# Performance work log

Measured on AMD Instinct MI355X. Metric: run time of the kernel, lower is better.

Reference implementation:

```python
import jax, jax.numpy as jnp
import numpy as np
from jax import lax

IMG_SIZE = 608
STRIDE = 32
NUM_CLASSES = 20
CONF_THRESH = 0.001
NMS_THRESH = 0.6
SLOPE = 0.1
B = 16
P5 = 512
FMP = IMG_SIZE // STRIDE   # 19
N = FMP * FMP              # 361 boxes per image


def _conv(x, w, b):
    y = lax.conv_general_dilated(x, w, (1, 1), 'SAME',
                                 dimension_numbers=('NCHW', 'OIHW', 'NCHW'))
    return y + b[None, :, None, None]


def _conv_act(x, w, b):
    # Conv block (conv + folded-BN bias + LeakyReLU(0.1)) at inference
    return jax.nn.leaky_relu(_conv(x, w, b), SLOPE)


def _grid():
    gy, gx = jnp.meshgrid(jnp.arange(FMP), jnp.arange(FMP), indexing='ij')
    return jnp.stack([gx, gy], axis=-1).reshape(-1, 2).astype(jnp.float32)  # [N,2]


def _decode(reg):
    # reg: [B,N,4] raw head output -> normalized x1y1x2y2 clamped to [0,1]
    xy = jax.nn.sigmoid(reg[..., :2]) + _grid()[None]          # center_sample=False
    wh = jnp.exp(reg[..., 2:])
    box = jnp.concatenate([xy - wh * 0.5, xy + wh * 0.5], axis=-1)
    return jnp.clip(box * (STRIDE / IMG_SIZE), 0.0, 1.0)


def _nms_one_class(boxes, s):
    # boxes: [N,4]; s: [N] scores with -1 marking boxes not of this class / below conf
    order = jnp.argsort(-s)
    b = boxes[order]
    valid = s[order] >= CONF_THRESH
    x1, y1, x2, y2 = b[:, 0], b[:, 1], b[:, 2], b[:, 3]
    areas = (x2 - x1) * (y2 - y1)
    w = jnp.maximum(1e-28, jnp.minimum(x2[:, None], x2[None, :]) - jnp.maximum(x1[:, None], x1[None, :]))
    h = jnp.maximum(1e-28, jnp.minimum(y2[:, None], y2[None, :]) - jnp.maximum(y1[:, None], y1[None, :]))
    inter = w * h
    iou = inter / (areas[:, None] + areas[None, :] - inter + 1e-14)  # [N,N]
    later = jnp.arange(N)[None, :] > jnp.arange(N)[:, None]
    sup = (iou > NMS_THRESH) & later

    def body(i, keep):
        # box i suppresses later boxes only if itself still kept (greedy NMS)
        return keep & ~(sup[i] & keep[i])

    keep = lax.fori_loop(0, N, body, valid)
    return jnp.zeros(N, dtype=bool).at[order].set(keep)  # back to original order


def _postprocess(boxes, scores):
    # per image: boxes [N,4], scores [N,C]
    cls_inds = jnp.argmax(scores, axis=-1)
    sc = jnp.max(scores, axis=-1)
    cmask = (cls_inds[None, :] == jnp.arange(NUM_CLASSES)[:, None]) & (sc >= CONF_THRESH)[None, :]
    masked = jnp.where(cmask, sc[None, :], -1.0)  # [C,N]
    keep_c = jax.vmap(_nms_one_class, in_axes=(None, 0))(boxes, masked)
    return sc, cls_inds, jnp.any(keep_c, axis=0)


def setup_inputs() -> dict:
    key = jax.random.key(0)
    ks = jax.random.split(key, 16)
    inp = {'x': jax.random.normal(ks[0], (B, P5, FMP, FMP), jnp.float32)}
    names = ['cls1', 'cls2', 'reg1', 'reg2', 'reg3', 'reg4']
    for j, nm in enumerate(names):
        inp['w_' + nm] = jax.random.normal(ks[1 + j], (P5, P5, 3, 3), jnp.float32) * 0.02
        inp['b_' + nm] = jnp.zeros((P5,), jnp.float32)
    inp['w_obj'] = jax.random.normal(ks[8], (1, P5, 1, 1), jnp.float32) * 0.01
    inp['b_obj'] = jnp.zeros((1,), jnp.float32)
    inp['w_clsh'] = jax.random.normal(ks[9], (NUM_CLASSES, P5, 1, 1), jnp.float32) * 0.01
    inp['b_clsh'] = jnp.zeros((NUM_CLASSES,), jnp.float32)
    inp['w_regh'] = jax.random.normal(ks[10], (4, P5, 1, 1), jnp.float32) * 0.01
    inp['b_regh'] = jnp.zeros((4,), jnp.float32)
    return inp


def reference(x, w_cls1, b_cls1, w_cls2, b_cls2, w_reg1, b_reg1, w_reg2, b_reg2,
              w_reg3, b_reg3, w_reg4, b_reg4, w_obj, b_obj, w_clsh, b_clsh,
              w_regh, b_regh):
    cf = _conv_act(_conv_act(x, w_cls1, b_cls1), w_cls2, b_cls2)
    rf = x
    for wv, bv in ((w_reg1, b_reg1), (w_reg2, b_reg2), (w_reg3, b_reg3), (w_reg4, b_reg4)):
        rf = _conv_act(rf, wv, bv)

    def flat(t):  # [B,C,H,W] -> [B,N,C]
        return t.reshape(t.shape[0], t.shape[1], -1).transpose(0, 2, 1)

    obj = flat(_conv(rf, w_obj, b_obj))      # [B,N,1]
    clsp = flat(_conv(cf, w_clsh, b_clsh))   # [B,N,C]
    regp = flat(_conv(rf, w_regh, b_regh))   # [B,N,4]

    boxes = _decode(regp)                                        # [B,N,4]
    scores = jax.nn.sigmoid(obj) * jax.nn.softmax(clsp, axis=-1)  # [B,N,C]
    sc, cls_inds, keep = jax.vmap(_postprocess)(boxes, scores)
    # fixed-shape outputs: boxes [B,N,4], per-box best score [B,N],
    # class index [B,N], NMS keep mask [B,N]
    return boxes, sc, cls_inds, keep
```

## Files before the change

### kernel.cpp

```cpp
#include <hip/hip_runtime.h>
#include <hip/hip_bf16.h>
#include <stdint.h>

typedef __bf16 bf16x8 __attribute__((ext_vector_type(8)));
typedef float  f32x16 __attribute__((ext_vector_type(16)));

#define FMPX 19
#define NPOS 361
#define CCH  512
#define NB   16
#define NCLS 20
#define CONF_T 0.001f
#define NMS_TH 0.6f
#define BSCALE (32.0f/608.0f)

#define SC_OFF   (NB*NPOS*4)
#define CLS_OFF  (SC_OFF + NB*NPOS)
#define KEEP_OFF (CLS_OFF + NB*NPOS)

#define GSTR  3528
#define PLANE ((size_t)3612672)
#define WSL   294912
#define XBUF  16384
#define WOFF  32768
#define SMEMB 51200

__device__ __forceinline__ void gl_lds16(const void* g, void* l) {
  __builtin_amdgcn_global_load_lds(
      (const __attribute__((address_space(1))) unsigned int*)g,
      (__attribute__((address_space(3))) unsigned int*)l, 16, 0, 0);
}
#define MFMA32(A,B,C) __builtin_amdgcn_mfma_f32_32x32x16_bf16(A,B,C,0,0,0)
#define SG(m,n) __builtin_amdgcn_sched_group_barrier(m, n, 0)
#define PRIO1 __builtin_amdgcn_s_setprio(1)
#define PRIO0 __builtin_amdgcn_s_setprio(0)

__global__ void split_x_k(const float* __restrict__ x, __bf16* __restrict__ Xd) {
  __shared__ float sx[8][368];
  int g = blockIdx.x, b = blockIdx.y;
  int tid = threadIdx.x;
  for (int i = tid; i < 8*361; i += 256) {
    int ci = i / 361, p = i - ci*361;
    sx[ci][p] = x[((size_t)b*CCH + g*8 + ci)*NPOS + p];
  }
  __syncthreads();
  for (int row = tid; row < 441; row += 256) {
    int y = row/21, xx = row - y*21;
    bf16x8 oh = {}, om = {};
    if (y >= 1 && y <= 19 && xx >= 1 && xx <= 19) {
      int p = (y-1)*19 + xx - 1;
#pragma unroll
      for (int j = 0; j < 8; ++j) {
        float v = sx[j][p];
        __bf16 hh = (__bf16)v;
        oh[j] = hh; om[j] = (__bf16)(v - (float)hh);
      }
    }
    size_t o = (((size_t)b)*64 + g)*GSTR + (size_t)row*8;
    *(bf16x8*)(Xd + o)         = oh;
    *(bf16x8*)(Xd + PLANE + o) = om;
  }
}

__global__ void repack_k(const float* __restrict__ w, __bf16* __restrict__ Wg) {
  __shared__ float sw[32][145];
  int slice = blockIdx.x, chunk = blockIdx.y;
  int tid = threadIdx.x;
  for (int i = tid; i < 32*144; i += 256) {
    int cl = i / 144, r = i - cl*144;
    sw[cl][r] = w[((size_t)slice*32 + cl)*4608 + chunk*144 + r];
  }
  __syncthreads();
  for (int u = tid; u < 1152; u += 256) {
    int co = u & 31, kh = (u >> 5) & 1, pt = u >> 6;
    int tap = pt % 9, pl = pt / 9;
    bf16x8 o;
#pragma unroll
    for (int j = 0; j < 8; ++j) {
      float v = sw[co][(kh*8 + j)*9 + tap];
      __bf16 hh = (__bf16)v;
      o[j] = pl == 0 ? hh : (__bf16)(v - (float)hh);
    }
    *(bf16x8*)(Wg + (((size_t)(slice*2 + pl)*9 + tap)*32 + chunk)*512 + kh*256 + co*8) = o;
  }
}

#define RD4X(SP, AT, IMM) do { \
  SP##0 = *(const bf16x8*)(Xc + AT##0 + (IMM)); \
  SP##1 = *(const bf16x8*)(Xc + AT##1 + (IMM)); \
  SP##2 = *(const bf16x8*)(Xc + AT##2 + (IMM)); \
  SP##3 = *(const bf16x8*)(Xc + AT##3 + (IMM)); } while (0)

#define CL4(SP, BH_, BM_) do { \
  acc0 = MFMA32(SP##0, BH_, acc0); acc1 = MFMA32(SP##1, BH_, acc1); \
  acc2 = MFMA32(SP##2, BH_, acc2); acc3 = MFMA32(SP##3, BH_, acc3); \
  acc0 = MFMA32(SP##0, BM_, acc0); acc1 = MFMA32(SP##1, BM_, acc1); \
  acc2 = MFMA32(SP##2, BM_, acc2); acc3 = MFMA32(SP##3, BM_, acc3); } while (0)

#define CL4H(SP, B_) do { \
  acc0 = MFMA32(SP##0, B_, acc0); acc1 = MFMA32(SP##1, B_, acc1); \
  acc2 = MFMA32(SP##2, B_, acc2); acc3 = MFMA32(SP##3, B_, acc3); } while (0)

#define STO(A, MTL) do { _Pragma("unroll") \
  for (int r = 0; r < 16; ++r) { \
    Lf[wq*2368 + ((MTL)*32 + 4*kh + (r & 3) + 8*(r >> 2))*37 + col] = (A)[r]; } } while (0)

__global__ __launch_bounds__(256, 3) void conv3x3_mfma(
    const __bf16* __restrict__ Xs, const __bf16* __restrict__ Wg,
    const float* __restrict__ bias, __bf16* __restrict__ Xd)
{
  __shared__ __attribute__((aligned(16))) char smem[SMEMB];
  const int tid = threadIdx.x;
  const int bid = blockIdx.x;
  const int b = bid & 15, slice = (bid >> 4) & 15, h = bid >> 8;
  const int lane = tid & 63;
  const int wq = __builtin_amdgcn_readfirstlane(tid >> 6);
  const int col = lane & 31, kh = lane >> 5;
  const int kh4096 = kh*4096;
  const int PB = h*128, CNT = (h == 2) ? 105 : 128;
  const int PEND = PB + CNT - 1;
  const int wstart = (h == 0) ? 0 : (h == 1) ? 140 : 282;
  const int clampU = (h == 2) ? 158 : 255;

  int ab0, ab1, ab2, ab3;
  {
    int ao[4];
#pragma unroll
    for (int mt = 0; mt < 4; ++mt) {
      int p = PB + mt*32 + col; if (p > PEND) p = PEND;
      int pp = p + 2*(p/19) + 22;
      ao[mt] = (pp - wstart)*16;
    }
    ab0 = ao[0]; ab1 = ao[1]; ab2 = ao[2]; ab3 = ao[3];
  }
  const int boff = kh*512 + col*16;

  const int goffs[9] = {-352,-336,-320,-16,0,16,320,336,352};
  const int t0 = 2*wq, t1 = t0 + 1;
  const int g0 = goffs[t0], g1 = goffs[t1];
  const int a8im = 352 + ((wq & 2) ? 8192 : 0);
  const int t0a0 = ab0+g0, t0a1 = ab1+g0, t0a2 = ab2+g0, t0a3 = ab3+g0;
  const int t1a0 = ab0+g1, t1a1 = ab1+g1, t1a2 = ab2+g1, t1a3 = ab3+g1;
  const int t8a0 = ab0+a8im, t8a1 = ab1+a8im, t8a2 = ab2+a8im, t8a3 = ab3+a8im;
  const int wb0 = t0*1024 + boff, wb1 = t1*1024 + boff;
  const int wb8 = 8192 + boff + ((wq & 1) ? 9216 : 0);

  int ux = wq*64 + lane; if (ux > clampU) ux = clampU;
  const __bf16* xsb = Xs + (size_t)b*64*GSTR + (size_t)(wstart + ux)*8;
  const __bf16* wsb = Wg + (size_t)slice*WSL + (size_t)lane*8;
  int wsrc0, wsrc1, wsrc2, wsrc3, wsrc4;
  int wdst0, wdst1, wdst2, wdst3, wdst4;
  {
    int ws[5], wd[5];
#pragma unroll
    for (int q = 0; q < 5; ++q) {
      int wk = (wq*5 + q) % 18;
      int pl = wk > 8 ? 1 : 0, tap = wk - 9*pl;
      ws[q] = ((pl*9 + tap)*32)*512;
      wd[q] = WOFF + pl*9216 + tap*1024;
    }
    wsrc0 = ws[0]; wsrc1 = ws[1]; wsrc2 = ws[2]; wsrc3 = ws[3]; wsrc4 = ws[4];
    wdst0 = wd[0]; wdst1 = wd[1]; wdst2 = wd[2]; wdst3 = wd[3]; wdst4 = wd[4];
  }

  auto stage = [&](int c1, int buf) {
    const __bf16* xs = xsb + (size_t)(2*c1)*GSTR;
    char* xd = smem + (buf ? XBUF : 0) + wq*1024;
    gl_lds16(xs,                    xd);
    gl_lds16(xs + GSTR,             xd + 4096);
    gl_lds16(xs + PLANE,            xd + 8192);
    gl_lds16(xs + PLANE + GSTR,     xd + 12288);
    const __bf16* wsc = wsb + (size_t)c1*512;
    gl_lds16(wsc + wsrc0, smem + wdst0);
    gl_lds16(wsc + wsrc1, smem + wdst1);
    gl_lds16(wsc + wsrc2, smem + wdst2);
    gl_lds16(wsc + wsrc3, smem + wdst3);
    gl_lds16(wsc + wsrc4, smem + wdst4);
  };

  f32x16 acc0 = {}, acc1 = {}, acc2 = {}, acc3 = {};

  stage(0, 0);
  __syncthreads();

  for (int c = 0; c < 32; ++c) {
    const char* Xc = smem + (c & 1)*XBUF + kh4096;
    const char* Wc = smem + WOFF;
    const int cn = (c < 31) ? (c + 1) : 31;

    bf16x8 B0h = *(const bf16x8*)(Wc + wb0);
    bf16x8 B0m = *(const bf16x8*)(Wc + wb0 + 9216);
    bf16x8 B1h = *(const bf16x8*)(Wc + wb1);
    bf16x8 B1m = *(const bf16x8*)(Wc + wb1 + 9216);
    bf16x8 B8v = *(const bf16x8*)(Wc + wb8);
    __syncthreads();

    stage(cn, (c + 1) & 1);

    bf16x8 Aa0, Aa1, Aa2, Aa3;
    bf16x8 Ab0, Ab1, Ab2, Ab3;
    PRIO1;
    RD4X(Aa, t0a, 0);
    RD4X(Ab, t0a, 8192);
    CL4(Aa, B0h, B0m);
    RD4X(Aa, t1a, 0);
    CL4(Ab, B0h, B0m);
    RD4X(Ab, t1a, 8192);
    CL4(Aa, B1h, B1m);
    RD4X(Aa, t8a, 0);
    CL4(Ab, B1h, B1m);
    CL4H(Aa, B8v);
    PRIO0;

    SG(0x100, 8);
    SG(0x70, 9);
#pragma unroll
    for (int i = 0; i < 4; ++i) { SG(8, 2); SG(0x100, 1); }
#pragma unroll
    for (int i = 0; i < 4; ++i) { SG(8, 2); SG(0x100, 1); }
#pragma unroll
    for (int i = 0; i < 4; ++i) { SG(8, 2); SG(0x100, 1); }
    SG(8, 12);
    __syncthreads();
  }

  float* Lf = (float*)smem;
#pragma unroll
  for (int half = 0; half < 2; ++half) {
    if (half == 0) { STO(acc0, 0); STO(acc1, 1); }
    else           { STO(acc2, 0); STO(acc3, 1); }
    __syncthreads();
    for (int u = tid; u < 512; u += 256) {
      int pl = u / 256, rem = u - pl*256;
      int gq = rem / 64, lp = rem - gq*64;
      int lpos = half*64 + lp;
      if (lpos < CNT) {
        int p = PB + lpos;
        int pp = p + 2*(p/19) + 22;
        const float* bb = bias + slice*32 + gq*8;
        bf16x8 o;
#pragma unroll
        for (int j = 0; j < 8; ++j) {
          int coix = lp*37 + gq*8 + j;
          float v = Lf[coix] + Lf[2368 + coix] + Lf[4736 + coix] + Lf[7104 + coix] + bb[j];
          v = v > 0.f ? v : 0.1f*v;
          __bf16 hh = (__bf16)v;
          o[j] = pl == 0 ? hh : (__bf16)(v - (float)hh);
        }
        *(bf16x8*)(Xd + (((size_t)pl*16 + b)*64 + slice*4 + gq)*GSTR + (size_t)pp*8) = o;
      }
    }
    __syncthreads();
  }

  if (h == 0) {
    for (int u = tid; u < 8*80; u += 256) {
      int pl = u / 320; int rem = u - pl*320;
      int gq = rem / 80; int ci2 = rem - gq*80;
      int rowpos;
      if (ci2 < 21) rowpos = ci2;
      else if (ci2 < 42) rowpos = 420 + (ci2 - 21);
      else { int q = ci2 - 42; rowpos = (1 + (q >> 1))*21 + 20*(q & 1); }
      bf16x8 z = {};
      *(bf16x8*)(Xd + (((size_t)pl*16 + b)*64 + slice*4 + gq)*GSTR + (size_t)rowpos*8) = z;
    }
  }
}

__global__ __launch_bounds__(256) void head_rf_k(
    const __bf16* __restrict__ F, const float* __restrict__ wobj,
    const float* __restrict__ bobj, const float* __restrict__ wreg,
    const float* __restrict__ breg, float* __restrict__ obj, float* __restrict__ regp)
{
  int gw = blockIdx.x*4 + (threadIdx.x >> 6);
  if (gw >= NB*NPOS) return;
  int lane = threadIdx.x & 63;
  int b = gw / NPOS, p = gw % NPOS;
  int pp = p + 2*(p/19) + 22;
  const __bf16* base = F + (((size_t)b)*64 + lane)*GSTR + (size_t)pp*8;
  bf16x8 v0 = *(const bf16x8*)base;
  bf16x8 v1 = *(const bf16x8*)(base + PLANE);
  float f[8];
#pragma unroll
  for (int j = 0; j < 8; ++j) f[j] = (float)v0[j] + (float)v1[j];
#pragma unroll
  for (int o = 0; o < 5; ++o) {
    const float* wp = (o == 0) ? wobj : wreg + (o-1)*CCH;
    float4 wa = *(const float4*)(wp + lane*8);
    float4 wb = *(const float4*)(wp + lane*8 + 4);
    float s2 = f[0]*wa.x + f[1]*wa.y + f[2]*wa.z + f[3]*wa.w
             + f[4]*wb.x + f[5]*wb.y + f[6]*wb.z + f[7]*wb.w;
#pragma unroll
    for (int d = 32; d; d >>= 1) s2 += __shfl_xor(s2, d);
    if (lane == 0) {
      if (o == 0) obj[gw] = s2 + bobj[0];
      else regp[(size_t)gw*4 + (o-1)] = s2 + breg[o-1];
    }
  }
}

__global__ __launch_bounds__(256) void head_cls_k(
    const __bf16* __restrict__ F, const float* __restrict__ wcls,
    const float* __restrict__ bcls, float* __restrict__ clsp)
{
  int gw = blockIdx.x*4 + (threadIdx.x >> 6);
  if (gw >= NB*NPOS) return;
  int lane = threadIdx.x & 63;
  int b = gw / NPOS, p = gw % NPOS;
  int pp = p + 2*(p/19) + 22;
  const __bf16* base = F + (((size_t)b)*64 + lane)*GSTR + (size_t)pp*8;
  bf16x8 v0 = *(const bf16x8*)base;
  bf16x8 v1 = *(const bf16x8*)(base + PLANE);
  float f[8];
#pragma unroll
  for (int j = 0; j < 8; ++j) f[j] = (float)v0[j] + (float)v1[j];
#pragma unroll
  for (int o = 0; o < NCLS; ++o) {
    const float* wp = wcls + o*CCH;
    float4 wa = *(const float4*)(wp + lane*8);
    float4 wb = *(const float4*)(wp + lane*8 + 4);
    float s2 = f[0]*wa.x + f[1]*wa.y + f[2]*wa.z + f[3]*wa.w
             + f[4]*wb.x + f[5]*wb.y + f[6]*wb.z + f[7]*wb.w;
#pragma unroll
    for (int d = 32; d; d >>= 1) s2 += __shfl_xor(s2, d);
    if (lane == 0) clsp[(size_t)gw*NCLS + o] = s2 + bcls[o];
  }
}

__global__ void decode_k(const float* __restrict__ obj, const float* __restrict__ clsp,
                         const float* __restrict__ regp, float* __restrict__ outb)
{
  int i = blockIdx.x * 256 + threadIdx.x;
  if (i >= NB * NPOS) return;
  int p = i % NPOS;
  float gx = (float)(p % FMPX), gy = (float)(p / FMPX);
  float4 rg = *(const float4*)&regp[(size_t)i * 4];
  float cx = 1.f / (1.f + expf(-rg.x)) + gx;
  float cy = 1.f / (1.f + expf(-rg.y)) + gy;
  float whw = expf(rg.z), whh = expf(rg.w);
  float x1 = fminf(fmaxf((cx - whw * 0.5f) * BSCALE, 0.f), 1.f);
  float y1 = fminf(fmaxf((cy - whh * 0.5f) * BSCALE, 0.f), 1.f);
  float x2 = fminf(fmaxf((cx + whw * 0.5f) * BSCALE, 0.f), 1.f);
  float y2 = fminf(fmaxf((cy + whh * 0.5f) * BSCALE, 0.f), 1.f);
  outb[(size_t)i * 4 + 0] = x1; outb[(size_t)i * 4 + 1] = y1;
  outb[(size_t)i * 4 + 2] = x2; outb[(size_t)i * 4 + 3] = y2;

  float so = 1.f / (1.f + expf(-obj[i]));
  float cv[20];
  const float4* cp = (const float4*)&clsp[(size_t)i * 20];
#pragma unroll
  for (int q = 0; q < 5; q++) {
    float4 v4 = cp[q];
    cv[q * 4] = v4.x; cv[q * 4 + 1] = v4.y; cv[q * 4 + 2] = v4.z; cv[q * 4 + 3] = v4.w;
  }
  float mx = cv[0];
#pragma unroll
  for (int c = 1; c < 20; c++) mx = fmaxf(mx, cv[c]);
  float sum = 0.f;
#pragma unroll
  for (int c = 0; c < 20; c++) { cv[c] = expf(cv[c] - mx); sum += cv[c]; }
  float inv = so / sum;
  float best = -1.f; int bi = 0;
#pragma unroll
  for (int c = 0; c < 20; c++) { float s = cv[c] * inv; if (s > best) { best = s; bi = c; } }
  outb[SC_OFF + i] = best;
  outb[CLS_OFF + i] = (float)bi;
  outb[KEEP_OFF + i] = 0.f;
}

__device__ inline unsigned ordf(float f) {
  unsigned u = __float_as_uint(f);
  return (u & 0x80000000u) ? ~u : (u | 0x80000000u);
}

__global__ __launch_bounds__(64) void nms_k(const float* __restrict__ outb, float* __restrict__ keep_out)
{
  int b = blockIdx.x / NCLS, c = blockIdx.x % NCLS;
  int lane = threadIdx.x;
  __shared__ unsigned long long keys[512];
  __shared__ float bx1[384], by1[384], bx2[384], by2[384], bar[384];
  __shared__ unsigned kp[384];
  __shared__ int sj[384];

  for (int i = lane; i < 512; i += 64) {
    unsigned long long key = 0ULL;
    if (i < NPOS) {
      float sc = outb[SC_OFF + b * NPOS + i];
      int ci = (int)outb[CLS_OFF + b * NPOS + i];
      float s = (ci == c && sc >= CONF_T) ? sc : -1.0f;
      key = ((unsigned long long)ordf(s) << 32) | (unsigned)(~(unsigned)i);
    }
    keys[i] = key;
  }
  __syncthreads();
  for (int kk = 2; kk <= 512; kk <<= 1) {
    for (int jj = kk >> 1; jj > 0; jj >>= 1) {
      for (int i = lane; i < 512; i += 64) {
        int l2 = i ^ jj;
        if (l2 > i) {
          unsigned long long a = keys[i], bb2 = keys[l2];
          bool dir = (i & kk) == 0;
          bool sw = dir ? (a < bb2) : (a > bb2);
          if (sw) { keys[i] = bb2; keys[l2] = a; }
        }
      }
      __syncthreads();
    }
  }
  unsigned ordc = ordf(CONF_T);
  int nvalid = 0;
  for (int i = lane; i < 384; i += 64) {
    unsigned long long key = keys[i];
    unsigned hi = (unsigned)(key >> 32);
    int j = (int)(~(unsigned)key);
    bool valid = (key != 0ULL) && (hi >= ordc);
    kp[i] = valid ? 1u : 0u;
    if (valid) {
      const float* bp = &outb[(size_t)(b * NPOS + j) * 4];
      float x1 = bp[0], y1 = bp[1], x2 = bp[2], y2 = bp[3];
      bx1[i] = x1; by1[i] = y1; bx2[i] = x2; by2[i] = y2;
      bar[i] = (x2 - x1) * (y2 - y1);
      sj[i] = j;
    } else { bx1[i] = 0; by1[i] = 0; bx2[i] = 0; by2[i] = 0; bar[i] = 0; sj[i] = 0; }
    nvalid += __popcll(__ballot(valid));
  }
  __syncthreads();
  for (int i = 0; i < nvalid; ++i) {
    if (kp[i]) {
      float x1i = bx1[i], y1i = by1[i], x2i = bx2[i], y2i = by2[i], ai = bar[i];
      for (int j2 = i + 1 + lane; j2 < nvalid; j2 += 64) {
        if (kp[j2]) {
          float ww = fmaxf(1e-28f, fminf(x2i, bx2[j2]) - fmaxf(x1i, bx1[j2]));
          float hh = fmaxf(1e-28f, fminf(y2i, by2[j2]) - fmaxf(y1i, by1[j2]));
          float inter = ww * hh;
          float iou = inter / (ai + bar[j2] - inter + 1e-14f);
          if (iou > NMS_TH) kp[j2] = 0u;
        }
      }
    }
    __syncthreads();
  }
  for (int i = lane; i < 384; i += 64)
    if (kp[i]) keep_out[b * NPOS + sj[i]] = 1.0f;
}

extern "C" void kernel_launch(void* const* d_in, const int* in_sizes, int n_in,
                              void* d_out, int out_size, void* d_ws, size_t ws_size,
                              hipStream_t stream)
{
  const float* x      = (const float*)d_in[0];
  const float* w_cls1 = (const float*)d_in[1];  const float* b_cls1 = (const float*)d_in[2];
  const float* w_cls2 = (const float*)d_in[3];  const float* b_cls2 = (const float*)d_in[4];
  const float* w_reg1 = (const float*)d_in[5];  const float* b_reg1 = (const float*)d_in[6];
  const float* w_reg2 = (const float*)d_in[7];  const float* b_reg2 = (const float*)d_in[8];
  const float* w_reg3 = (const float*)d_in[9];  const float* b_reg3 = (const float*)d_in[10];
  const float* w_reg4 = (const float*)d_in[11]; const float* b_reg4 = (const float*)d_in[12];
  const float* w_obj  = (const float*)d_in[13]; const float* b_obj  = (const float*)d_in[14];
  const float* w_clsh = (const float*)d_in[15]; const float* b_clsh = (const float*)d_in[16];
  const float* w_regh = (const float*)d_in[17]; const float* b_regh = (const float*)d_in[18];
  float* outb = (float*)d_out;

  __bf16* Xs0 = (__bf16*)d_ws;
  __bf16* XsA = Xs0 + 2*PLANE;
  __bf16* XsB = XsA + 2*PLANE;
  __bf16* Wg  = XsB + 2*PLANE;
  float* obj  = (float*)(Wg + (size_t)16*WSL);
  float* regp = obj + NB*NPOS;
  float* clsp = regp + (size_t)NB*NPOS*4;

  auto conv = [&](const float* wsrc, const float* bsrc, const __bf16* src, __bf16* dst) {
    repack_k<<<dim3(16, 32), 256, 0, stream>>>(wsrc, Wg);
    conv3x3_mfma<<<768, 256, 0, stream>>>(src, Wg, bsrc, dst);
  };

  split_x_k<<<dim3(64, NB), 256, 0, stream>>>(x, Xs0);
  conv(w_reg1, b_reg1, Xs0, XsA);
  conv(w_reg2, b_reg2, XsA, XsB);
  conv(w_reg3, b_reg3, XsB, XsA);
  conv(w_reg4, b_reg4, XsA, XsB);
  head_rf_k<<<1444, 256, 0, stream>>>(XsB, w_obj, b_obj, w_regh, b_regh, obj, regp);
  conv(w_cls1, b_cls1, Xs0, XsA);
  conv(w_cls2, b_cls2, XsA, XsB);
  head_cls_k<<<1444, 256, 0, stream>>>(XsB, w_clsh, b_clsh, clsp);
  decode_k<<<(NB * NPOS + 255) / 256, 256, 0, stream>>>(obj, clsp, regp, outb);
  nms_k<<<NB * NCLS, 64, 0, stream>>>(outb, outb + KEEP_OFF);
}
```

Before: 710.9 us.

## Retile conv3x3 MFMA to 96 positions by 64 output channels per block

The 3x3 conv kernel now computes 64 output channels over 96 spatial positions per block instead of 32 channels over 128 positions. This doubles reuse of each staged input tile across output channels and cuts the grid from 768 to 512 blocks, with six accumulators per wave instead of four. Weight repacking is changed to match the new slice layout and loads with float4. The cost is more LDS per block (68 KB), more registers, and occupancy lowered from 3 to 2 blocks per CU.

```diff
diff --git a/kernel.cpp b/kernel.cpp
--- a/kernel.cpp
+++ b/kernel.cpp
@@ -20,10 +20,10 @@
 
 #define GSTR  3528
 #define PLANE ((size_t)3612672)
-#define WSL   294912
+#define WSL   589824
 #define XBUF  16384
 #define WOFF  32768
-#define SMEMB 51200
+#define SMEMB 69632
 
 __device__ __forceinline__ void gl_lds16(const void* g, void* l) {
   __builtin_amdgcn_global_load_lds(
@@ -63,104 +63,105 @@
 }
 
 __global__ void repack_k(const float* __restrict__ w, __bf16* __restrict__ Wg) {
-  __shared__ float sw[32][145];
+  __shared__ float sw[64][148];
   int slice = blockIdx.x, chunk = blockIdx.y;
   int tid = threadIdx.x;
-  for (int i = tid; i < 32*144; i += 256) {
-    int cl = i / 144, r = i - cl*144;
-    sw[cl][r] = w[((size_t)slice*32 + cl)*4608 + chunk*144 + r];
+  for (int i = tid; i < 64*36; i += 256) {
+    int cl = i / 36, fq = i - cl*36;
+    ((float4*)&sw[cl][0])[fq] =
+      ((const float4*)(w + (size_t)(slice*64 + cl)*4608 + (size_t)chunk*144))[fq];
   }
   __syncthreads();
-  for (int u = tid; u < 1152; u += 256) {
-    int co = u & 31, kh = (u >> 5) & 1, pt = u >> 6;
+  for (int u = tid; u < 2304; u += 256) {
+    int co = u & 63, rest = u >> 6;
+    int khh = rest & 1, pt = rest >> 1;
     int tap = pt % 9, pl = pt / 9;
     bf16x8 o;
 #pragma unroll
     for (int j = 0; j < 8; ++j) {
-      float v = sw[co][(kh*8 + j)*9 + tap];
+      float v = sw[co][(khh*8 + j)*9 + tap];
       __bf16 hh = (__bf16)v;
       o[j] = pl == 0 ? hh : (__bf16)(v - (float)hh);
     }
-    *(bf16x8*)(Wg + (((size_t)(slice*2 + pl)*9 + tap)*32 + chunk)*512 + kh*256 + co*8) = o;
-  }
-}
-
-#define RD4X(SP, AT, IMM) do { \
-  SP##0 = *(const bf16x8*)(Xc + AT##0 + (IMM)); \
-  SP##1 = *(const bf16x8*)(Xc + AT##1 + (IMM)); \
-  SP##2 = *(const bf16x8*)(Xc + AT##2 + (IMM)); \
-  SP##3 = *(const bf16x8*)(Xc + AT##3 + (IMM)); } while (0)
-
-#define CL4(SP, BH_, BM_) do { \
-  acc0 = MFMA32(SP##0, BH_, acc0); acc1 = MFMA32(SP##1, BH_, acc1); \
-  acc2 = MFMA32(SP##2, BH_, acc2); acc3 = MFMA32(SP##3, BH_, acc3); \
-  acc0 = MFMA32(SP##0, BM_, acc0); acc1 = MFMA32(SP##1, BM_, acc1); \
-  acc2 = MFMA32(SP##2, BM_, acc2); acc3 = MFMA32(SP##3, BM_, acc3); } while (0)
-
-#define CL4H(SP, B_) do { \
-  acc0 = MFMA32(SP##0, B_, acc0); acc1 = MFMA32(SP##1, B_, acc1); \
-  acc2 = MFMA32(SP##2, B_, acc2); acc3 = MFMA32(SP##3, B_, acc3); } while (0)
+    *(bf16x8*)(Wg + (size_t)slice*WSL + (size_t)pt*32768 + chunk*1024 + khh*512 + co*8) = o;
+  }
+}
+
+#define RD3(SP, A0_, A1_, A2_, IMM) do { \
+  SP##0 = *(const bf16x8*)(Xc + (A0_) + (IMM)); \
+  SP##1 = *(const bf16x8*)(Xc + (A1_) + (IMM)); \
+  SP##2 = *(const bf16x8*)(Xc + (A2_) + (IMM)); } while (0)
+
+#define CL12(S, BH0_, BH1_, BM0_, BM1_) do { \
+  a00 = MFMA32(S##0, BH0_, a00); a01 = MFMA32(S##0, BH1_, a01); \
+  a10 = MFMA32(S##1, BH0_, a10); a11 = MFMA32(S##1, BH1_, a11); \
+  a20 = MFMA32(S##2, BH0_, a20); a21 = MFMA32(S##2, BH1_, a21); \
+  a00 = MFMA32(S##0, BM0_, a00); a01 = MFMA32(S##0, BM1_, a01); \
+  a10 = MFMA32(S##1, BM0_, a10); a11 = MFMA32(S##1, BM1_, a11); \
+  a20 = MFMA32(S##2, BM0_, a20); a21 = MFMA32(S##2, BM1_, a21); } while (0)
+
+#define CL6(S, B0_, B1_) do { \
+  a00 = MFMA32(S##0, B0_, a00); a01 = MFMA32(S##0, B1_, a01); \
+  a10 = MFMA32(S##1, B0_, a10); a11 = MFMA32(S##1, B1_, a11); \
+  a20 = MFMA32(S##2, B0_, a20); a21 = MFMA32(S##2, B1_, a21); } while (0)
 
 #define STO(A, MTL) do { _Pragma("unroll") \
   for (int r = 0; r < 16; ++r) { \
-    Lf[wq*2368 + ((MTL)*32 + 4*kh + (r & 3) + 8*(r >> 2))*37 + col] = (A)[r]; } } while (0)
-
-__global__ __launch_bounds__(256, 3) void conv3x3_mfma(
+    Lf[wq*3168 + ((MTL)*32 + 4*kh + (r & 3) + 8*(r >> 2))*33 + col] = (A)[r]; } } while (0)
+
+__global__ __launch_bounds__(256, 2) void conv3x3_mfma(
     const __bf16* __restrict__ Xs, const __bf16* __restrict__ Wg,
     const float* __restrict__ bias, __bf16* __restrict__ Xd)
 {
   __shared__ __attribute__((aligned(16))) char smem[SMEMB];
   const int tid = threadIdx.x;
   const int bid = blockIdx.x;
-  const int b = bid & 15, slice = (bid >> 4) & 15, h = bid >> 8;
+  const int b = bid & 15, slice = (bid >> 4) & 7, q = bid >> 7;
   const int lane = tid & 63;
   const int wq = __builtin_amdgcn_readfirstlane(tid >> 6);
   const int col = lane & 31, kh = lane >> 5;
   const int kh4096 = kh*4096;
-  const int PB = h*128, CNT = (h == 2) ? 105 : 128;
+  const int PB = q*96, CNT = (q == 3) ? 73 : 96;
   const int PEND = PB + CNT - 1;
-  const int wstart = (h == 0) ? 0 : (h == 1) ? 140 : 282;
-  const int clampU = (h == 2) ? 158 : 255;
-
-  int ab0, ab1, ab2, ab3;
+  const int wstart = q*106;
+  int cu0 = 440 - wstart; const int clampU = cu0 > 255 ? 255 : cu0;
+
+  int ab0, ab1, ab2;
   {
-    int ao[4];
-#pragma unroll
-    for (int mt = 0; mt < 4; ++mt) {
+    int ao[3];
+#pragma unroll
+    for (int mt = 0; mt < 3; ++mt) {
       int p = PB + mt*32 + col; if (p > PEND) p = PEND;
       int pp = p + 2*(p/19) + 22;
       ao[mt] = (pp - wstart)*16;
     }
-    ab0 = ao[0]; ab1 = ao[1]; ab2 = ao[2]; ab3 = ao[3];
-  }
-  const int boff = kh*512 + col*16;
+    ab0 = ao[0]; ab1 = ao[1]; ab2 = ao[2];
+  }
 
   const int goffs[9] = {-352,-336,-320,-16,0,16,320,336,352};
   const int t0 = 2*wq, t1 = t0 + 1;
   const int g0 = goffs[t0], g1 = goffs[t1];
-  const int a8im = 352 + ((wq & 2) ? 8192 : 0);
-  const int t0a0 = ab0+g0, t0a1 = ab1+g0, t0a2 = ab2+g0, t0a3 = ab3+g0;
-  const int t1a0 = ab0+g1, t1a1 = ab1+g1, t1a2 = ab2+g1, t1a3 = ab3+g1;
-  const int t8a0 = ab0+a8im, t8a1 = ab1+a8im, t8a2 = ab2+a8im, t8a3 = ab3+a8im;
-  const int wb0 = t0*1024 + boff, wb1 = t1*1024 + boff;
-  const int wb8 = 8192 + boff + ((wq & 1) ? 9216 : 0);
+  const int t0a0 = ab0+g0, t0a1 = ab1+g0, t0a2 = ab2+g0;
+  const int t1a0 = ab0+g1, t1a1 = ab1+g1, t1a2 = ab2+g1;
+  const int a8im = 352 + ((wq >> 1) ? 8192 : 0);
+  const int t8a0 = ab0+a8im, t8a1 = ab1+a8im, t8a2 = ab2+a8im;
+  const int bbase = kh*1024 + col*16;
+  const int wbT0h = t0*2048 + bbase;
+  const int wbT0m = (9 + t0)*2048 + bbase;
+  const int wbT1h = t1*2048 + bbase;
+  const int wbT1m = (9 + t1)*2048 + bbase;
+  const int wb8v  = ((wq & 1)*9 + 8)*2048 + bbase;
 
   int ux = wq*64 + lane; if (ux > clampU) ux = clampU;
   const __bf16* xsb = Xs + (size_t)b*64*GSTR + (size_t)(wstart + ux)*8;
   const __bf16* wsb = Wg + (size_t)slice*WSL + (size_t)lane*8;
-  int wsrc0, wsrc1, wsrc2, wsrc3, wsrc4;
-  int wdst0, wdst1, wdst2, wdst3, wdst4;
-  {
-    int ws[5], wd[5];
-#pragma unroll
-    for (int q = 0; q < 5; ++q) {
-      int wk = (wq*5 + q) % 18;
-      int pl = wk > 8 ? 1 : 0, tap = wk - 9*pl;
-      ws[q] = ((pl*9 + tap)*32)*512;
-      wd[q] = WOFF + pl*9216 + tap*1024;
-    }
-    wsrc0 = ws[0]; wsrc1 = ws[1]; wsrc2 = ws[2]; wsrc3 = ws[3]; wsrc4 = ws[4];
-    wdst0 = wd[0]; wdst1 = wd[1]; wdst2 = wd[2]; wdst3 = wd[3]; wdst4 = wd[4];
+  int wsrc[9], wdst[9];
+#pragma unroll
+  for (int qi = 0; qi < 9; ++qi) {
+    int k = wq*9 + qi;
+    int pt = k >> 1, half = k & 1;
+    wsrc[qi] = pt*32768 + half*512;
+    wdst[qi] = WOFF + pt*2048 + half*1024;
   }
 
   auto stage = [&](int c1, int buf) {
@@ -170,99 +171,101 @@
     gl_lds16(xs + GSTR,             xd + 4096);
     gl_lds16(xs + PLANE,            xd + 8192);
     gl_lds16(xs + PLANE + GSTR,     xd + 12288);
-    const __bf16* wsc = wsb + (size_t)c1*512;
-    gl_lds16(wsc + wsrc0, smem + wdst0);
-    gl_lds16(wsc + wsrc1, smem + wdst1);
-    gl_lds16(wsc + wsrc2, smem + wdst2);
-    gl_lds16(wsc + wsrc3, smem + wdst3);
-    gl_lds16(wsc + wsrc4, smem + wdst4);
+    const __bf16* wsc = wsb + (size_t)c1*1024;
+#pragma unroll
+    for (int qi = 0; qi < 9; ++qi)
+      gl_lds16(wsc + wsrc[qi], smem + wdst[qi]);
   };
 
-  f32x16 acc0 = {}, acc1 = {}, acc2 = {}, acc3 = {};
+  f32x16 a00 = {}, a01 = {}, a10 = {}, a11 = {}, a20 = {}, a21 = {};
 
   stage(0, 0);
   __syncthreads();
 
+  const char* Wc = smem + WOFF;
   for (int c = 0; c < 32; ++c) {
     const char* Xc = smem + (c & 1)*XBUF + kh4096;
-    const char* Wc = smem + WOFF;
     const int cn = (c < 31) ? (c + 1) : 31;
 
-    bf16x8 B0h = *(const bf16x8*)(Wc + wb0);
-    bf16x8 B0m = *(const bf16x8*)(Wc + wb0 + 9216);
-    bf16x8 B1h = *(const bf16x8*)(Wc + wb1);
-    bf16x8 B1m = *(const bf16x8*)(Wc + wb1 + 9216);
-    bf16x8 B8v = *(const bf16x8*)(Wc + wb8);
+    bf16x8 B0h0 = *(const bf16x8*)(Wc + wbT0h);
+    bf16x8 B0h1 = *(const bf16x8*)(Wc + wbT0h + 512);
+    bf16x8 B0m0 = *(const bf16x8*)(Wc + wbT0m);
+    bf16x8 B0m1 = *(const bf16x8*)(Wc + wbT0m + 512);
+    bf16x8 B1h0 = *(const bf16x8*)(Wc + wbT1h);
+    bf16x8 B1h1 = *(const bf16x8*)(Wc + wbT1h + 512);
+    bf16x8 B1m0 = *(const bf16x8*)(Wc + wbT1m);
+    bf16x8 B1m1 = *(const bf16x8*)(Wc + wbT1m + 512);
+    bf16x8 B8n0 = *(const bf16x8*)(Wc + wb8v);
+    bf16x8 B8n1 = *(const bf16x8*)(Wc + wb8v + 512);
     __syncthreads();
 
     stage(cn, (c + 1) & 1);
 
-    bf16x8 Aa0, Aa1, Aa2, Aa3;
-    bf16x8 Ab0, Ab1, Ab2, Ab3;
+    bf16x8 Aa0, Aa1, Aa2, Ab0, Ab1, Ab2, Ac0, Ac1, Ac2;
+    bf16x8 Ad0, Ad1, Ad2, Ae0, Ae1, Ae2;
     PRIO1;
-    RD4X(Aa, t0a, 0);
-    RD4X(Ab, t0a, 8192);
-    CL4(Aa, B0h, B0m);
-    RD4X(Aa, t1a, 0);
-    CL4(Ab, B0h, B0m);
-    RD4X(Ab, t1a, 8192);
-    CL4(Aa, B1h, B1m);
-    RD4X(Aa, t8a, 0);
-    CL4(Ab, B1h, B1m);
-    CL4H(Aa, B8v);
+    RD3(Aa, t0a0, t0a1, t0a2, 0);
+    RD3(Ab, t0a0, t0a1, t0a2, 8192);
+    RD3(Ac, t1a0, t1a1, t1a2, 0);
+    RD3(Ad, t1a0, t1a1, t1a2, 8192);
+    RD3(Ae, t8a0, t8a1, t8a2, 0);
+    CL12(Aa, B0h0, B0h1, B0m0, B0m1);
+    CL12(Ab, B0h0, B0h1, B0m0, B0m1);
+    CL12(Ac, B1h0, B1h1, B1m0, B1m1);
+    CL12(Ad, B1h0, B1h1, B1m0, B1m1);
+    CL6(Ae, B8n0, B8n1);
     PRIO0;
 
-    SG(0x100, 8);
-    SG(0x70, 9);
-#pragma unroll
-    for (int i = 0; i < 4; ++i) { SG(8, 2); SG(0x100, 1); }
-#pragma unroll
-    for (int i = 0; i < 4; ++i) { SG(8, 2); SG(0x100, 1); }
-#pragma unroll
-    for (int i = 0; i < 4; ++i) { SG(8, 2); SG(0x100, 1); }
-    SG(8, 12);
+    SG(0x100, 6);
+    SG(0x70, 13);
+    SG(0x100, 6);
+    SG(8, 4); SG(0x100, 1);
+    SG(8, 4); SG(0x100, 1);
+    SG(8, 4); SG(0x100, 1);
+    SG(8, 42);
     __syncthreads();
   }
 
   float* Lf = (float*)smem;
 #pragma unroll
   for (int half = 0; half < 2; ++half) {
-    if (half == 0) { STO(acc0, 0); STO(acc1, 1); }
-    else           { STO(acc2, 0); STO(acc3, 1); }
+    if (half == 0) { STO(a00, 0); STO(a10, 1); STO(a20, 2); }
+    else           { STO(a01, 0); STO(a11, 1); STO(a21, 2); }
     __syncthreads();
-    for (int u = tid; u < 512; u += 256) {
-      int pl = u / 256, rem = u - pl*256;
-      int gq = rem / 64, lp = rem - gq*64;
-      int lpos = half*64 + lp;
-      if (lpos < CNT) {
-        int p = PB + lpos;
+    for (int u = tid; u < 768; u += 256) {
+      int pl = u / 384, rem = u - pl*384;
+      int gq = rem / 96, lp = rem - gq*96;
+      if (lp < CNT) {
+        int p = PB + lp;
         int pp = p + 2*(p/19) + 22;
-        const float* bb = bias + slice*32 + gq*8;
+        const float* bb = bias + slice*64 + half*32 + gq*8;
         bf16x8 o;
 #pragma unroll
         for (int j = 0; j < 8; ++j) {
-          int coix = lp*37 + gq*8 + j;
-          float v = Lf[coix] + Lf[2368 + coix] + Lf[4736 + coix] + Lf[7104 + coix] + bb[j];
+          int coix = lp*33 + gq*8 + j;
+          float v = Lf[coix] + Lf[3168 + coix] + Lf[6336 + coix] + Lf[9504 + coix] + bb[j];
           v = v > 0.f ? v : 0.1f*v;
           __bf16 hh = (__bf16)v;
           o[j] = pl == 0 ? hh : (__bf16)(v - (float)hh);
         }
-        *(bf16x8*)(Xd + (((size_t)pl*16 + b)*64 + slice*4 + gq)*GSTR + (size_t)pp*8) = o;
+        *(bf16x8*)(Xd + (((size_t)pl*16 + b)*64 + slice*8 + half*4 + gq)*GSTR
+                      + (size_t)pp*8) = o;
       }
     }
     __syncthreads();
   }
 
-  if (h == 0) {
-    for (int u = tid; u < 8*80; u += 256) {
-      int pl = u / 320; int rem = u - pl*320;
-      int gq = rem / 80; int ci2 = rem - gq*80;
+  if (q == 0) {
+    for (int u = tid; u < 1280; u += 256) {
+      int pl = u / 640; int rem = u - pl*640;
+      int gl = rem / 80; int ci2 = rem - gl*80;
       int rowpos;
       if (ci2 < 21) rowpos = ci2;
       else if (ci2 < 42) rowpos = 420 + (ci2 - 21);
-      else { int q = ci2 - 42; rowpos = (1 + (q >> 1))*21 + 20*(q & 1); }
+      else { int q2 = ci2 - 42; rowpos = (1 + (q2 >> 1))*21 + 20*(q2 & 1); }
       bf16x8 z = {};
-      *(bf16x8*)(Xd + (((size_t)pl*16 + b)*64 + slice*4 + gq)*GSTR + (size_t)rowpos*8) = z;
+      *(bf16x8*)(Xd + (((size_t)pl*16 + b)*64 + slice*8 + gl)*GSTR
+                    + (size_t)rowpos*8) = z;
     }
   }
 }
@@ -464,13 +467,13 @@
   __bf16* XsA = Xs0 + 2*PLANE;
   __bf16* XsB = XsA + 2*PLANE;
   __bf16* Wg  = XsB + 2*PLANE;
-  float* obj  = (float*)(Wg + (size_t)16*WSL);
+  float* obj  = (float*)(Wg + (size_t)8*WSL);
   float* regp = obj + NB*NPOS;
   float* clsp = regp + (size_t)NB*NPOS*4;
 
   auto conv = [&](const float* wsrc, const float* bsrc, const __bf16* src, __bf16* dst) {
-    repack_k<<<dim3(16, 32), 256, 0, stream>>>(wsrc, Wg);
-    conv3x3_mfma<<<768, 256, 0, stream>>>(src, Wg, bsrc, dst);
+    repack_k<<<dim3(8, 32), 256, 0, stream>>>(wsrc, Wg);
+    conv3x3_mfma<<<512, 256, 0, stream>>>(src, Wg, bsrc, dst);
   };
 
   split_x_k<<<dim3(64, NB), 256, 0, stream>>>(x, Xs0);
```

Result: no change. 720.6 us (+1.4%).
